# Optimization experiments

Hardware: AMD Instinct MI355X
Metric: run time of the kernel (lower is better)

The kernel has to match this reference:

```python
import math
import jax, jax.numpy as jnp
import numpy as np

B, N, M = 8, 2048, 1024
INPUT_SIZE = 512
HEAD_DIM = 64
NUM_HEADS = 6
ATTN_SIZE = HEAD_DIM * NUM_HEADS
MAX_CLASSES = 512


def setup_inputs() -> dict:
    key = jax.random.key(0)
    k1, k2, k3, k4, k5, k6, k7 = jax.random.split(key, 7)
    bound = 1.0 / math.sqrt(INPUT_SIZE)
    return {
        "train_embeddings": jax.random.normal(k1, (B, N, INPUT_SIZE), jnp.float32),
        "test_embeddings": jax.random.normal(k2, (B, M, INPUT_SIZE), jnp.float32),
        "targets": jax.random.randint(k3, (B, N), 0, MAX_CLASSES),
        # torch nn.Linear weights, stored as [in, out] for direct matmul
        "Wq": jax.random.uniform(k4, (INPUT_SIZE, ATTN_SIZE), jnp.float32, -bound, bound),
        "bq": jax.random.uniform(k5, (ATTN_SIZE,), jnp.float32, -bound, bound),
        "Wk": jax.random.uniform(k6, (INPUT_SIZE, ATTN_SIZE), jnp.float32, -bound, bound),
        "bk": jax.random.uniform(k7, (ATTN_SIZE,), jnp.float32, -bound, bound),
    }


def reference(train_embeddings, test_embeddings, targets, Wq, bq, Wk, bk):
    b, m, _ = test_embeddings.shape
    # projections -> [B, S, H, D]
    q_bmhd = (test_embeddings @ Wq + bq).reshape(b, m, NUM_HEADS, HEAD_DIM)
    k_bnhd = (train_embeddings @ Wk + bk).reshape(b, -1, NUM_HEADS, HEAD_DIM)
    scale = 1.0 / math.sqrt(HEAD_DIM)  # SDPA default scale
    # attention scores [B, H, M, N]
    scores = jnp.einsum("bmhd,bnhd->bhmn", q_bmhd, k_bnhd) * scale
    attn = jax.nn.softmax(scores, axis=-1)
    # one-hot train targets [B, N, C]; chunk-folding in the torch code is a
    # memory trick — mathematically it is just attn @ one_hot per head
    onehot_bnc = jax.nn.one_hot(targets, MAX_CLASSES, dtype=q_bmhd.dtype)
    out_bhmc = jnp.einsum("bhmn,bnc->bhmc", attn, onehot_bnc)
    out_bmc = out_bhmc.mean(axis=1)          # mean over heads
    out_mbc = out_bmc.transpose(1, 0, 2)      # [M, B, C]
    return jnp.log(jnp.clip(out_mbc, 1e-05) + 3e-05)
```

## Files before the change

kernel.cpp:

```cpp
#include <hip/hip_runtime.h>
#include <hip/hip_bf16.h>

#define BQ 8
#define NN 2048
#define MM 1024
#define EE 512
#define NH 6
#define AA 384
#define CC 512

#define KROW_B (AA * 2)
#define TILE_B (16 * KROW_B)
#define STILE_B (32 * KROW_B)
#define WROW_B (EE * 2)
#define WTILE_B (16 * WROW_B)

#define QSCALE 0.1803368801111204f

typedef __bf16 bf16x8 __attribute__((ext_vector_type(8)));
typedef float  f32x4  __attribute__((ext_vector_type(4)));
using bf16 = __hip_bfloat16;

static __device__ __forceinline__ f32x4 mfma16(bf16x8 a, bf16x8 b, f32x4 c) {
  return __builtin_amdgcn_mfma_f32_16x16x32_bf16(a, b, c, 0, 0, 0);
}

typedef __attribute__((address_space(1))) const void gconst_void;
typedef __attribute__((address_space(3))) void lds_void_t;
static __device__ __forceinline__ void ld_lds16(const void* g, void* l) {
  __builtin_amdgcn_global_load_lds((gconst_void*)g, (lds_void_t*)l, 16, 0, 0);
}

static __device__ __forceinline__ unsigned short f2bfu(float x) {
  union { __hip_bfloat16 h; unsigned short u; } v;
  v.h = __float2bfloat16(x);
  return v.u;
}
static __device__ __forceinline__ float bf2f(unsigned short u) {
  union { unsigned int i; float f; } x;
  x.i = ((unsigned int)u) << 16;
  return x.f;
}

__global__ __launch_bounds__(512) void prep_kernel(
    const float* __restrict__ Wq, const float* __restrict__ Wk,
    bf16* __restrict__ WqT, bf16* __restrict__ WkT,
    const int* __restrict__ targets, int* __restrict__ offs, int* __restrict__ idxs)
{
  __shared__ float t[64][65];
  __shared__ int cnt[CC], ssum[CC], pos[CC];
  int bid = blockIdx.x, tid = threadIdx.x;
  if (bid < 96) {
    if (tid >= 256) { __syncthreads(); __syncthreads(); return; }
    int id = bid;
    const float* W = (id < 48) ? Wq : Wk;
    bf16* WT = (id < 48) ? WqT : WkT;
    if (id >= 48) id -= 48;
    int kb = (id / 6) * 64, nb = (id % 6) * 64;
    int lr = tid >> 4, lc = (tid & 15) * 4;
    #pragma unroll
    for (int p = 0; p < 4; p++) {
      int k = lr + p * 16;
      float4 v = *reinterpret_cast<const float4*>(W + (size_t)(kb + k) * AA + nb + lc);
      t[k][lc] = v.x; t[k][lc + 1] = v.y; t[k][lc + 2] = v.z; t[k][lc + 3] = v.w;
    }
    __syncthreads();
    #pragma unroll
    for (int p = 0; p < 4; p++) {
      int n = lr + p * 16;
      bf16* dst = WT + (size_t)(nb + n) * EE + kb + lc;
      dst[0] = __float2bfloat16(t[lc][n]);
      dst[1] = __float2bfloat16(t[lc + 1][n]);
      dst[2] = __float2bfloat16(t[lc + 2][n]);
      dst[3] = __float2bfloat16(t[lc + 3][n]);
    }
    __syncthreads();
    return;
  }
  int b = bid - 96;
  cnt[tid] = 0;
  __syncthreads();
  int tv[4];
  #pragma unroll
  for (int i = 0; i < 4; i++) {
    tv[i] = targets[b * NN + tid * 4 + i];
    atomicAdd(&cnt[tv[i]], 1);
  }
  __syncthreads();
  ssum[tid] = cnt[tid];
  __syncthreads();
  for (int d = 1; d < CC; d <<= 1) {
    int v = (tid >= d) ? ssum[tid - d] : 0;
    __syncthreads();
    ssum[tid] += v;
    __syncthreads();
  }
  int excl = ssum[tid] - cnt[tid];
  offs[b * (CC + 1) + tid] = excl;
  if (tid == CC - 1) offs[b * (CC + 1) + CC] = NN;
  pos[tid] = excl;
  __syncthreads();
  #pragma unroll
  for (int i = 0; i < 4; i++) {
    int p = atomicAdd(&pos[tv[i]], 1);
    idxs[b * NN + p] = tid * 4 + i;
  }
}

__global__ __launch_bounds__(256, 3) void proj_kernel(
    const float* __restrict__ test, const float* __restrict__ train,
    const bf16* __restrict__ WqT, const bf16* __restrict__ WkT,
    const float* __restrict__ bq, const float* __restrict__ bk,
    const int* __restrict__ idxs,
    bf16* __restrict__ Qb, bf16* __restrict__ Kb)
{
  __shared__ char wbuf[3][WTILE_B];
  int tid = threadIdx.x, wid = tid >> 6, lane = tid & 63;
  int bid = blockIdx.x;
  int sub = bid & 1, unit = bid >> 1;
  const bf16* WT; const float* bias; bf16* C; float scale; int m0;
  const float* arow;
  int row = lane & 15, hi = lane >> 4;
  if (unit < 128) {
    WT = WqT; bias = bq; C = Qb; scale = QSCALE; m0 = unit * 64 + wid * 16;
    arow = test + (size_t)(m0 + row) * EE + hi * 8;
  } else {
    WT = WkT; bias = bk; C = Kb; scale = 1.0f;
    int g0 = (unit - 128) * 64 + wid * 16;
    m0 = g0;
    int g = g0 + row;
    int b = g >> 11, pos = g & (NN - 1);
    int srcrow = idxs[b * NN + pos];
    arow = train + ((size_t)b * NN + srcrow) * EE + hi * 8;
  }

  bf16x8 af[16];
  #pragma unroll
  for (int ks = 0; ks < 16; ks++) {
    float4 u = *reinterpret_cast<const float4*>(arow + ks * 32);
    float4 v = *reinterpret_cast<const float4*>(arow + ks * 32 + 4);
    bf16x8 f;
    f[0] = (__bf16)u.x; f[1] = (__bf16)u.y; f[2] = (__bf16)u.z; f[3] = (__bf16)u.w;
    f[4] = (__bf16)v.x; f[5] = (__bf16)v.y; f[6] = (__bf16)v.z; f[7] = (__bf16)v.w;
    af[ks] = f;
  }

  int ldso[4], srco[4];
  #pragma unroll
  for (int i = 0; i < 4; i++) {
    int off = tid * 16 + i * 4096;
    int rw = off >> 10, c = off & 1023;
    ldso[i] = off;
    srco[i] = rw * WROW_B + (c ^ ((rw & 7) << 4));
  }
  const char* wgbase = (const char*)WT + (size_t)sub * 12 * WTILE_B;
  int sw = (row & 7) << 4;

  auto stage = [&](int t, int buf) {
    const char* src = wgbase + (size_t)t * WTILE_B;
    #pragma unroll
    for (int i = 0; i < 4; i++) ld_lds16(src + srco[i], wbuf[buf] + ldso[i]);
  };
  auto compute = [&](int buf, int t) {
    const char* wb = wbuf[buf] + row * WROW_B;
    f32x4 acc0 = {0.f, 0.f, 0.f, 0.f}, acc1 = {0.f, 0.f, 0.f, 0.f};
    #pragma unroll
    for (int ks = 0; ks < 16; ks += 2) {
      bf16x8 w0 = *reinterpret_cast<const bf16x8*>(wb + ((hi * 16 + ks * 64) ^ sw));
      bf16x8 w1 = *reinterpret_cast<const bf16x8*>(wb + ((hi * 16 + (ks + 1) * 64) ^ sw));
      acc0 = mfma16(af[ks], w0, acc0);
      acc1 = mfma16(af[ks + 1], w1, acc1);
    }
    f32x4 acc = acc0 + acc1;
    int ocol = (sub * 12 + t) * 16 + row;
    float bv = bias[ocol];
    #pragma unroll
    for (int j = 0; j < 4; j++)
      C[(size_t)(m0 + hi * 4 + j) * AA + ocol] = __float2bfloat16((acc[j] + bv) * scale);
  };

  stage(0, 0);
  stage(1, 1);
  asm volatile("s_waitcnt vmcnt(4)" ::: "memory");
  __builtin_amdgcn_s_barrier();
  __builtin_amdgcn_sched_barrier(0);
  stage(2, 2);
  compute(0, 0);

  int cur = 1, stg = 0;
  #pragma unroll 1
  for (int t = 1; t < 11; t++) {
    asm volatile("s_waitcnt vmcnt(8)" ::: "memory");
    __builtin_amdgcn_s_barrier();
    __builtin_amdgcn_sched_barrier(0);
    if (t < 10) stage(t + 2, stg);
    compute(cur, t);
    cur = cur + 1 < 3 ? cur + 1 : 0;
    stg = stg + 1 < 3 ? stg + 1 : 0;
  }
  asm volatile("s_waitcnt vmcnt(4)" ::: "memory");
  __builtin_amdgcn_s_barrier();
  __builtin_amdgcn_sched_barrier(0);
  compute(cur, 11);
}

__global__ __launch_bounds__(256, 2) void zpass_kernel(
    const bf16* __restrict__ Qb, const bf16* __restrict__ Kb, float* __restrict__ Zp)
{
  __shared__ char kbuf[2][STILE_B];
  int id = blockIdx.x;
  int b = id & 7, r = id >> 3, mt = r & 7, nc = r >> 3;
  int tid = threadIdx.x, wid = tid >> 6, lane = tid & 63;
  int m0 = mt * 128 + wid * 32, n0 = nc * 256;
  int row = lane & 15, hi = lane >> 4;

  bf16x8 qf[2][12];
  #pragma unroll
  for (int s = 0; s < 2; s++) {
    const bf16* qrow = Qb + ((size_t)(b * MM + m0 + s * 16 + row)) * AA + hi * 8;
    #pragma unroll
    for (int ks = 0; ks < 12; ks++) qf[s][ks] = *reinterpret_cast<const bf16x8*>(qrow + ks * 32);
  }

  int ldso[6], srco[6];
  #pragma unroll
  for (int i = 0; i < 6; i++) {
    int off = tid * 16 + i * 4096;
    int rw = off / KROW_B, c = off - rw * KROW_B;
    ldso[i] = off;
    srco[i] = rw * KROW_B + (c ^ ((rw & 7) << 4));
  }
  const char* kgbase = (const char*)(Kb + ((size_t)(b * NN + n0)) * AA);

  int sw = (row & 7) << 4;
  int rbase = row * KROW_B;
  int x0 = rbase + ((hi * 16) ^ sw);
  int x1 = rbase + (((hi * 16) + 64) ^ sw);

  float zacc[2][NH][4];
  #pragma unroll
  for (int s = 0; s < 2; s++)
    #pragma unroll
    for (int h = 0; h < NH; h++)
      #pragma unroll
      for (int j = 0; j < 4; j++) zacc[s][h][j] = 0.f;

  auto stage = [&](int t, int buf) {
    const char* src = kgbase + (size_t)t * STILE_B;
    #pragma unroll
    for (int i = 0; i < 6; i++) ld_lds16(src + srco[i], kbuf[buf] + ldso[i]);
  };
  auto compute = [&](int buf) {
    __builtin_amdgcn_s_setprio(1);
    #pragma unroll
    for (int sub = 0; sub < 2; sub++) {
      const char* kb = kbuf[buf] + sub * TILE_B;
      #pragma unroll
      for (int h = 0; h < NH; h++) {
        bf16x8 k0 = *reinterpret_cast<const bf16x8*>(kb + h * 128 + x0);
        bf16x8 k1 = *reinterpret_cast<const bf16x8*>(kb + h * 128 + x1);
        f32x4 a0 = {0.f, 0.f, 0.f, 0.f}, a1 = {0.f, 0.f, 0.f, 0.f};
        a0 = mfma16(qf[0][2 * h], k0, a0);
        a1 = mfma16(qf[1][2 * h], k0, a1);
        a0 = mfma16(qf[0][2 * h + 1], k1, a0);
        a1 = mfma16(qf[1][2 * h + 1], k1, a1);
        #pragma unroll
        for (int j = 0; j < 4; j++) {
          zacc[0][h][j] += __builtin_amdgcn_exp2f(a0[j]);
          zacc[1][h][j] += __builtin_amdgcn_exp2f(a1[j]);
        }
      }
    }
    __builtin_amdgcn_s_setprio(0);
  };

  stage(0, 0);
  asm volatile("s_waitcnt vmcnt(0)" ::: "memory");
  __builtin_amdgcn_s_barrier();
  __builtin_amdgcn_sched_barrier(0);
  stage(1, 1);
  compute(0);

  #pragma unroll 1
  for (int i = 1; i < 8; i++) {
    asm volatile("s_waitcnt vmcnt(0)" ::: "memory");
    __builtin_amdgcn_s_barrier();
    __builtin_amdgcn_sched_barrier(0);
    if (i < 7) stage(i + 1, (i + 1) & 1);
    compute(i & 1);
  }

  #pragma unroll
  for (int s = 0; s < 2; s++)
    #pragma unroll
    for (int h = 0; h < NH; h++)
      #pragma unroll
      for (int j = 0; j < 4; j++) {
        float v = zacc[s][h][j];
        v += __shfl_xor(v, 1); v += __shfl_xor(v, 2);
        v += __shfl_xor(v, 4); v += __shfl_xor(v, 8);
        zacc[s][h][j] = v;
      }
  if (row == 0) {
    #pragma unroll
    for (int s = 0; s < 2; s++)
      #pragma unroll
      for (int h = 0; h < NH; h++)
        #pragma unroll
        for (int j = 0; j < 4; j++)
          Zp[(((size_t)nc * 8 + b) * NH + h) * MM + m0 + s * 16 + hi * 4 + j] = zacc[s][h][j];
  }
}

__global__ __launch_bounds__(256, 2) void wpass_kernel(
    const bf16* __restrict__ Qb, const bf16* __restrict__ Kb,
    const float* __restrict__ Zp, bf16* __restrict__ W2)
{
  __shared__ char kbuf[2][STILE_B];
  int id = blockIdx.x;
  int b = id & 7, r = id >> 3, mt = r & 7, nc = r >> 3;
  int tid = threadIdx.x, wid = tid >> 6, lane = tid & 63;
  int m0 = mt * 128 + wid * 32, n0 = nc * 256;
  int row = lane & 15, hi = lane >> 4;

  bf16x8 qf[2][12];
  #pragma unroll
  for (int s = 0; s < 2; s++) {
    const bf16* qrow = Qb + ((size_t)(b * MM + m0 + s * 16 + row)) * AA + hi * 8;
    #pragma unroll
    for (int ks = 0; ks < 12; ks++) qf[s][ks] = *reinterpret_cast<const bf16x8*>(qrow + ks * 32);
  }

  f32x4 lrz4[2][NH];
  #pragma unroll
  for (int s = 0; s < 2; s++)
    #pragma unroll
    for (int h = 0; h < NH; h++) {
      f32x4 z = {0.f, 0.f, 0.f, 0.f};
      #pragma unroll
      for (int p = 0; p < 8; p++)
        z += *reinterpret_cast<const f32x4*>(Zp + (((size_t)p * 8 + b) * NH + h) * MM + m0 + s * 16 + hi * 4);
      f32x4 l;
      #pragma unroll
      for (int j = 0; j < 4; j++) l[j] = -__log2f(6.0f * z[j]);
      lrz4[s][h] = l;
    }

  int ldso[6], srco[6];
  #pragma unroll
  for (int i = 0; i < 6; i++) {
    int off = tid * 16 + i * 4096;
    int rw = off / KROW_B, c = off - rw * KROW_B;
    ldso[i] = off;
    srco[i] = rw * KROW_B + (c ^ ((rw & 7) << 4));
  }
  const char* kgbase = (const char*)(Kb + ((size_t)(b * NN + n0)) * AA);

  int sw = (row & 7) << 4;
  int rbase = row * KROW_B;
  int x0 = rbase + ((hi * 16) ^ sw);
  int x1 = rbase + (((hi * 16) + 64) ^ sw);

  int m4a = (m0 >> 2) + hi;
  int m4b = ((m0 + 16) >> 2) + hi;

  auto stage = [&](int t, int buf) {
    const char* src = kgbase + (size_t)t * STILE_B;
    #pragma unroll
    for (int i = 0; i < 6; i++) ld_lds16(src + srco[i], kbuf[buf] + ldso[i]);
  };
  auto compute = [&](int buf, int st) {
    #pragma unroll
    for (int sub = 0; sub < 2; sub++) {
      const char* kb = kbuf[buf] + sub * TILE_B;
      __builtin_amdgcn_s_setprio(1);
      float w0a = 0.f, w1a = 0.f, w2a = 0.f, w3a = 0.f;
      float w0b = 0.f, w1b = 0.f, w2b = 0.f, w3b = 0.f;
      #pragma unroll
      for (int h = 0; h < NH; h++) {
        bf16x8 k0 = *reinterpret_cast<const bf16x8*>(kb + h * 128 + x0);
        bf16x8 k1 = *reinterpret_cast<const bf16x8*>(kb + h * 128 + x1);
        f32x4 a0 = mfma16(qf[0][2 * h], k0, lrz4[0][h]);
        f32x4 a1 = mfma16(qf[1][2 * h], k0, lrz4[1][h]);
        a0 = mfma16(qf[0][2 * h + 1], k1, a0);
        a1 = mfma16(qf[1][2 * h + 1], k1, a1);
        w0a += __builtin_amdgcn_exp2f(a0[0]);
        w1a += __builtin_amdgcn_exp2f(a0[1]);
        w2a += __builtin_amdgcn_exp2f(a0[2]);
        w3a += __builtin_amdgcn_exp2f(a0[3]);
        w0b += __builtin_amdgcn_exp2f(a1[0]);
        w1b += __builtin_amdgcn_exp2f(a1[1]);
        w2b += __builtin_amdgcn_exp2f(a1[2]);
        w3b += __builtin_amdgcn_exp2f(a1[3]);
      }
      __builtin_amdgcn_s_setprio(0);
      int n = n0 + (st * 2 + sub) * 16 + row;
      ushort4 qa, qb2;
      qa.x = f2bfu(w0a); qa.y = f2bfu(w1a); qa.z = f2bfu(w2a); qa.w = f2bfu(w3a);
      qb2.x = f2bfu(w0b); qb2.y = f2bfu(w1b); qb2.z = f2bfu(w2b); qb2.w = f2bfu(w3b);
      *reinterpret_cast<ushort4*>((unsigned short*)W2 + (((size_t)(b * 256 + m4a)) * NN + n) * 4) = qa;
      *reinterpret_cast<ushort4*>((unsigned short*)W2 + (((size_t)(b * 256 + m4b)) * NN + n) * 4) = qb2;
    }
  };

  stage(0, 0);
  asm volatile("s_waitcnt vmcnt(0)" ::: "memory");
  __builtin_amdgcn_s_barrier();
  __builtin_amdgcn_sched_barrier(0);
  stage(1, 1);
  compute(0, 0);

  #pragma unroll 1
  for (int i = 1; i < 8; i++) {
    asm volatile("s_waitcnt vmcnt(4)" ::: "memory");
    __builtin_amdgcn_s_barrier();
    __builtin_amdgcn_sched_barrier(0);
    if (i < 7) stage(i + 1, (i + 1) & 1);
    compute(i & 1, i);
  }
}

__global__ __launch_bounds__(512) void gather_kernel(
    const bf16* __restrict__ W2, const int* __restrict__ offs, float* __restrict__ out)
{
  __shared__ char wl[2 * NN * 8];
  int id = blockIdx.x;
  int b = id & 7, mt = id >> 3;
  int g0 = mt * 2;
  int tid = threadIdx.x;

  const uint4* src = (const uint4*)((const unsigned short*)W2 + ((size_t)(b * 256 + g0)) * NN * 4);
  uint4* dst = (uint4*)wl;
  #pragma unroll
  for (int i = tid; i < 2 * NN * 8 / 16; i += 512) dst[i] = src[i];
  __syncthreads();

  int c = tid;
  int o0 = offs[b * (CC + 1) + c], o1 = offs[b * (CC + 1) + c + 1];
  #pragma unroll 1
  for (int g = 0; g < 2; g++) {
    const char* base = wl + g * (NN * 8);
    float s0 = 0.f, s1 = 0.f, s2 = 0.f, s3 = 0.f;
    #pragma unroll 1
    for (int i = o0; i < o1; i++) {
      ushort4 v = *reinterpret_cast<const ushort4*>(base + (size_t)i * 8);
      s0 += bf2f(v.x); s1 += bf2f(v.y); s2 += bf2f(v.z); s3 += bf2f(v.w);
    }
    int m = mt * 8 + g * 4;
    out[((size_t)(m + 0) * BQ + b) * CC + c] = __logf(fmaxf(s0, 1e-5f) + 3e-5f);
    out[((size_t)(m + 1) * BQ + b) * CC + c] = __logf(fmaxf(s1, 1e-5f) + 3e-5f);
    out[((size_t)(m + 2) * BQ + b) * CC + c] = __logf(fmaxf(s2, 1e-5f) + 3e-5f);
    out[((size_t)(m + 3) * BQ + b) * CC + c] = __logf(fmaxf(s3, 1e-5f) + 3e-5f);
  }
}

extern "C" void kernel_launch(void* const* d_in, const int* in_sizes, int n_in,
                              void* d_out, int out_size, void* d_ws, size_t ws_size,
                              hipStream_t stream) {
  const float* train = (const float*)d_in[0];
  const float* test  = (const float*)d_in[1];
  const int*   tgt   = (const int*)d_in[2];
  const float* Wq    = (const float*)d_in[3];
  const float* bq    = (const float*)d_in[4];
  const float* Wk    = (const float*)d_in[5];
  const float* bk    = (const float*)d_in[6];
  float* out = (float*)d_out;

  char* ws = (char*)d_ws;
  bf16*  WqT  = (bf16*)(ws);
  bf16*  WkT  = (bf16*)(ws + 393216);
  bf16*  Qb   = (bf16*)(ws + 786432);
  bf16*  Kb   = (bf16*)(ws + 7077888);
  float* Zp   = (float*)(ws + 19660800);
  bf16*  Wbuf = (bf16*)(ws + 21233664);
  int*   offs = (int*)(ws + 54788096);
  int*   idxs = (int*)(ws + 54804512);

  prep_kernel<<<104, 512, 0, stream>>>(Wq, Wk, WqT, WkT, tgt, offs, idxs);
  proj_kernel<<<768, 256, 0, stream>>>(test, train, WqT, WkT, bq, bk, idxs, Qb, Kb);
  zpass_kernel<<<512, 256, 0, stream>>>(Qb, Kb, Zp);
  wpass_kernel<<<512, 256, 0, stream>>>(Qb, Kb, Zp, Wbuf);
  gather_kernel<<<1024, 512, 0, stream>>>(Wbuf, offs, out);
}
```

Baseline: 103.7 us.

## Pack W2 as 8 bf16 per row for 16-byte stores and gathers

The intermediate W2 buffer is re-laid out so each entry holds 8 bf16 values (two 16-row m-subtiles) instead of 4. The wpass kernel then issues one 16-byte store per sub-tile instead of two 8-byte stores, and waits on fewer outstanding loads (vmcnt 2 instead of 4). The gather kernel handles 8 m values per block with a single pass over the class index range, reading 16-byte LDS entries, which halves the per-block loop overhead over targets. The zpass and wpass accumulators are vectorized, and the Z reduction writes directly. The gather grid mapping changes accordingly, and any mismatch in the m index mapping would give wrong output.

```diff
diff --git a/kernel.cpp b/kernel.cpp
--- a/kernel.cpp
+++ b/kernel.cpp
@@ -31,14 +31,14 @@
   __builtin_amdgcn_global_load_lds((gconst_void*)g, (lds_void_t*)l, 16, 0, 0);
 }
 
-static __device__ __forceinline__ unsigned short f2bfu(float x) {
+static __device__ __forceinline__ unsigned f2bfu(float x) {
   union { __hip_bfloat16 h; unsigned short u; } v;
   v.h = __float2bfloat16(x);
-  return v.u;
-}
-static __device__ __forceinline__ float bf2f(unsigned short u) {
+  return (unsigned)v.u;
+}
+static __device__ __forceinline__ float bf2f(unsigned u) {
   union { unsigned int i; float f; } x;
-  x.i = ((unsigned int)u) << 16;
+  x.i = u << 16;
   return x.f;
 }
 
@@ -237,13 +237,11 @@
   int x0 = rbase + ((hi * 16) ^ sw);
   int x1 = rbase + (((hi * 16) + 64) ^ sw);
 
-  float zacc[2][NH][4];
+  f32x4 zacc[2][NH];
   #pragma unroll
   for (int s = 0; s < 2; s++)
     #pragma unroll
-    for (int h = 0; h < NH; h++)
-      #pragma unroll
-      for (int j = 0; j < 4; j++) zacc[s][h][j] = 0.f;
+    for (int h = 0; h < NH; h++) zacc[s][h] = (f32x4){0.f, 0.f, 0.f, 0.f};
 
   auto stage = [&](int t, int buf) {
     const char* src = kgbase + (size_t)t * STILE_B;
@@ -264,11 +262,12 @@
         a1 = mfma16(qf[1][2 * h], k0, a1);
         a0 = mfma16(qf[0][2 * h + 1], k1, a0);
         a1 = mfma16(qf[1][2 * h + 1], k1, a1);
-        #pragma unroll
-        for (int j = 0; j < 4; j++) {
-          zacc[0][h][j] += __builtin_amdgcn_exp2f(a0[j]);
-          zacc[1][h][j] += __builtin_amdgcn_exp2f(a1[j]);
-        }
+        f32x4 e0 = { __builtin_amdgcn_exp2f(a0[0]), __builtin_amdgcn_exp2f(a0[1]),
+                     __builtin_amdgcn_exp2f(a0[2]), __builtin_amdgcn_exp2f(a0[3]) };
+        f32x4 e1 = { __builtin_amdgcn_exp2f(a1[0]), __builtin_amdgcn_exp2f(a1[1]),
+                     __builtin_amdgcn_exp2f(a1[2]), __builtin_amdgcn_exp2f(a1[3]) };
+        zacc[0][h] += e0;
+        zacc[1][h] += e1;
       }
     }
     __builtin_amdgcn_s_setprio(0);
@@ -299,17 +298,9 @@
         float v = zacc[s][h][j];
         v += __shfl_xor(v, 1); v += __shfl_xor(v, 2);
         v += __shfl_xor(v, 4); v += __shfl_xor(v, 8);
-        zacc[s][h][j] = v;
+        if (row == 0)
+          Zp[(((size_t)nc * 8 + b) * NH + h) * MM + m0 + s * 16 + hi * 4 + j] = v;
       }
-  if (row == 0) {
-    #pragma unroll
-    for (int s = 0; s < 2; s++)
-      #pragma unroll
-      for (int h = 0; h < NH; h++)
-        #pragma unroll
-        for (int j = 0; j < 4; j++)
-          Zp[(((size_t)nc * 8 + b) * NH + h) * MM + m0 + s * 16 + hi * 4 + j] = zacc[s][h][j];
-  }
 }
 
 __global__ __launch_bounds__(256, 2) void wpass_kernel(
@@ -361,8 +352,7 @@
   int x0 = rbase + ((hi * 16) ^ sw);
   int x1 = rbase + (((hi * 16) + 64) ^ sw);
 
-  int m4a = (m0 >> 2) + hi;
-  int m4b = ((m0 + 16) >> 2) + hi;
+  int G = ((m0 >> 5) << 2) + hi;
 
   auto stage = [&](int t, int buf) {
     const char* src = kgbase + (size_t)t * STILE_B;
@@ -374,8 +364,7 @@
     for (int sub = 0; sub < 2; sub++) {
       const char* kb = kbuf[buf] + sub * TILE_B;
       __builtin_amdgcn_s_setprio(1);
-      float w0a = 0.f, w1a = 0.f, w2a = 0.f, w3a = 0.f;
-      float w0b = 0.f, w1b = 0.f, w2b = 0.f, w3b = 0.f;
+      f32x4 wa0 = {0.f, 0.f, 0.f, 0.f}, wa1 = {0.f, 0.f, 0.f, 0.f};
       #pragma unroll
       for (int h = 0; h < NH; h++) {
         bf16x8 k0 = *reinterpret_cast<const bf16x8*>(kb + h * 128 + x0);
@@ -384,22 +373,21 @@
         f32x4 a1 = mfma16(qf[1][2 * h], k0, lrz4[1][h]);
         a0 = mfma16(qf[0][2 * h + 1], k1, a0);
         a1 = mfma16(qf[1][2 * h + 1], k1, a1);
-        w0a += __builtin_amdgcn_exp2f(a0[0]);
-        w1a += __builtin_amdgcn_exp2f(a0[1]);
-        w2a += __builtin_amdgcn_exp2f(a0[2]);
-        w3a += __builtin_amdgcn_exp2f(a0[3]);
-        w0b += __builtin_amdgcn_exp2f(a1[0]);
-        w1b += __builtin_amdgcn_exp2f(a1[1]);
-        w2b += __builtin_amdgcn_exp2f(a1[2]);
-        w3b += __builtin_amdgcn_exp2f(a1[3]);
+        f32x4 e0 = { __builtin_amdgcn_exp2f(a0[0]), __builtin_amdgcn_exp2f(a0[1]),
+                     __builtin_amdgcn_exp2f(a0[2]), __builtin_amdgcn_exp2f(a0[3]) };
+        f32x4 e1 = { __builtin_amdgcn_exp2f(a1[0]), __builtin_amdgcn_exp2f(a1[1]),
+                     __builtin_amdgcn_exp2f(a1[2]), __builtin_amdgcn_exp2f(a1[3]) };
+        wa0 += e0;
+        wa1 += e1;
       }
       __builtin_amdgcn_s_setprio(0);
       int n = n0 + (st * 2 + sub) * 16 + row;
-      ushort4 qa, qb2;
-      qa.x = f2bfu(w0a); qa.y = f2bfu(w1a); qa.z = f2bfu(w2a); qa.w = f2bfu(w3a);
-      qb2.x = f2bfu(w0b); qb2.y = f2bfu(w1b); qb2.z = f2bfu(w2b); qb2.w = f2bfu(w3b);
-      *reinterpret_cast<ushort4*>((unsigned short*)W2 + (((size_t)(b * 256 + m4a)) * NN + n) * 4) = qa;
-      *reinterpret_cast<ushort4*>((unsigned short*)W2 + (((size_t)(b * 256 + m4b)) * NN + n) * 4) = qb2;
+      uint4 stv;
+      stv.x = f2bfu(wa0[0]) | (f2bfu(wa0[1]) << 16);
+      stv.y = f2bfu(wa0[2]) | (f2bfu(wa0[3]) << 16);
+      stv.z = f2bfu(wa1[0]) | (f2bfu(wa1[1]) << 16);
+      stv.w = f2bfu(wa1[2]) | (f2bfu(wa1[3]) << 16);
+      *reinterpret_cast<uint4*>((unsigned short*)W2 + (((size_t)(b * 128 + G)) * NN + n) * 8) = stv;
     }
   };
 
@@ -412,7 +400,7 @@
 
   #pragma unroll 1
   for (int i = 1; i < 8; i++) {
-    asm volatile("s_waitcnt vmcnt(4)" ::: "memory");
+    asm volatile("s_waitcnt vmcnt(2)" ::: "memory");
     __builtin_amdgcn_s_barrier();
     __builtin_amdgcn_sched_barrier(0);
     if (i < 7) stage(i + 1, (i + 1) & 1);
@@ -423,34 +411,35 @@
 __global__ __launch_bounds__(512) void gather_kernel(
     const bf16* __restrict__ W2, const int* __restrict__ offs, float* __restrict__ out)
 {
-  __shared__ char wl[2 * NN * 8];
+  __shared__ char wl[NN * 16];
   int id = blockIdx.x;
-  int b = id & 7, mt = id >> 3;
-  int g0 = mt * 2;
+  int b = id & 7, g = id >> 3;
   int tid = threadIdx.x;
 
-  const uint4* src = (const uint4*)((const unsigned short*)W2 + ((size_t)(b * 256 + g0)) * NN * 4);
+  const uint4* src = (const uint4*)((const unsigned short*)W2 + ((size_t)(b * 128 + g)) * NN * 8);
   uint4* dst = (uint4*)wl;
   #pragma unroll
-  for (int i = tid; i < 2 * NN * 8 / 16; i += 512) dst[i] = src[i];
+  for (int i = tid; i < NN; i += 512) dst[i] = src[i];
   __syncthreads();
 
   int c = tid;
   int o0 = offs[b * (CC + 1) + c], o1 = offs[b * (CC + 1) + c + 1];
+  float s[8];
+  #pragma unroll
+  for (int k = 0; k < 8; k++) s[k] = 0.f;
   #pragma unroll 1
-  for (int g = 0; g < 2; g++) {
-    const char* base = wl + g * (NN * 8);
-    float s0 = 0.f, s1 = 0.f, s2 = 0.f, s3 = 0.f;
-    #pragma unroll 1
-    for (int i = o0; i < o1; i++) {
-      ushort4 v = *reinterpret_cast<const ushort4*>(base + (size_t)i * 8);
-      s0 += bf2f(v.x); s1 += bf2f(v.y); s2 += bf2f(v.z); s3 += bf2f(v.w);
-    }
-    int m = mt * 8 + g * 4;
-    out[((size_t)(m + 0) * BQ + b) * CC + c] = __logf(fmaxf(s0, 1e-5f) + 3e-5f);
-    out[((size_t)(m + 1) * BQ + b) * CC + c] = __logf(fmaxf(s1, 1e-5f) + 3e-5f);
-    out[((size_t)(m + 2) * BQ + b) * CC + c] = __logf(fmaxf(s2, 1e-5f) + 3e-5f);
-    out[((size_t)(m + 3) * BQ + b) * CC + c] = __logf(fmaxf(s3, 1e-5f) + 3e-5f);
+  for (int i = o0; i < o1; i++) {
+    uint4 v = *reinterpret_cast<const uint4*>(wl + (size_t)i * 16);
+    s[0] += bf2f(v.x & 0xFFFFu); s[1] += bf2f(v.x >> 16);
+    s[2] += bf2f(v.y & 0xFFFFu); s[3] += bf2f(v.y >> 16);
+    s[4] += bf2f(v.z & 0xFFFFu); s[5] += bf2f(v.z >> 16);
+    s[6] += bf2f(v.w & 0xFFFFu); s[7] += bf2f(v.w >> 16);
+  }
+  int mbase = (g >> 2) * 32 + (g & 3) * 4;
+  #pragma unroll
+  for (int k = 0; k < 8; k++) {
+    int m = mbase + (k >> 2) * 16 + (k & 3);
+    out[((size_t)m * BQ + b) * CC + c] = __logf(fmaxf(s[k], 1e-5f) + 3e-5f);
   }
 }
 
```

Result: slower. 108.6 us (+4.8%).
